# Kernel tuning notes

Hardware: AMD Instinct MI355X
Metric: run time of the kernel (lower is better)

The kernel has to match this reference:

```python
import jax, jax.numpy as jnp
import numpy as np

ALPHA, BETA, GAMMA, DELTA = 1.0, 1.0, 1.0, 0.001
DV, DD = 0.5, 1.5
N_INST = 8
EDGES_MAX = 512
EPS = 1e-12


def _safe_norm(sq):
    # sqrt of a sum-of-squares with a tiny eps for grad stability at 0
    return jnp.sqrt(jnp.maximum(sq, 0.0) + EPS)


def _per_image(feat, labels, label_edges):
    # feat: [P, C]; labels, label_edges: [P] int32 in [0, N_INST)
    P, C = feat.shape
    N = N_INST
    counts = jax.ops.segment_sum(jnp.ones((P,), feat.dtype), labels, num_segments=N)  # [N]
    means = jax.ops.segment_sum(feat, labels, num_segments=N) / counts[:, None]       # [N, C]

    # --- variance (pull) loss: per-pixel distance to its cluster mean ---
    d = _safe_norm(jnp.sum((feat - means[labels]) ** 2, axis=-1))  # [P]
    hinge = jax.nn.relu(d - DV) ** 2
    var_loss = jnp.sum(jax.ops.segment_sum(hinge, labels, num_segments=N) / counts) / N

    # --- distance (push) loss between cluster means, upper triangle ---
    diff = means[:, None, :] - means[None, :, :]
    dm = _safe_norm(jnp.sum(diff ** 2, axis=-1))  # [N, N]
    triu = jnp.triu(jnp.ones((N, N), dtype=bool), k=1)
    dist_loss = jnp.sum(jnp.where(triu, jax.nn.relu(2.0 * DD - dm) ** 2, 0.0)) / (N * (N - 1))

    # --- edge loss: first EDGES_MAX boundary pixels per instance (deterministic subsample) ---
    pix = jnp.arange(P, dtype=feat.dtype)
    def first_members(i):
        score = jnp.where(label_edges == i, -pix, -jnp.inf)
        _, idx = jax.lax.top_k(score, EDGES_MAX)
        return idx
    sel = jax.vmap(first_members)(jnp.arange(N))  # [N, E]
    eb = feat[sel.reshape(-1)]                    # [N*E, C]
    sq = jnp.sum(eb ** 2, axis=-1)
    d2 = sq[:, None] + sq[None, :] - 2.0 * (eb @ eb.T)  # [N*E, N*E] squared dists
    pd = _safe_norm(d2)
    pv = jax.nn.relu(2.0 * (DD - DV) - pd) ** 2
    pair = pv.reshape(N, EDGES_MAX, N, EDGES_MAX).sum(axis=(1, 3)) / (EDGES_MAX * EDGES_MAX)
    edge_loss = jnp.sum(jnp.where(triu, pair, 0.0)) / (N * (N - 1))

    # --- regularization on cluster means ---
    reg_loss = jnp.mean(_safe_norm(jnp.sum(means ** 2, axis=-1)))
    return var_loss, dist_loss, edge_loss, reg_loss


def setup_inputs() -> dict:
    key = jax.random.key(0)
    k1, k2, k3 = jax.random.split(key, 3)
    B, C, H, W = 4, 32, 512, 512
    features = jax.random.normal(k1, (B, C, H, W), jnp.float32)
    labels = jax.random.randint(k2, (B, H, W), 0, N_INST, jnp.int32)
    labelEdges = jax.random.randint(k3, (B, H, W), 0, N_INST, jnp.int32)
    return {"features": features, "labels": labels, "labelEdges": labelEdges}


def reference(features, labels, labelEdges):
    B, C, H, W = features.shape
    feat = features.transpose(0, 2, 3, 1).reshape(B, H * W, C)
    lab = labels.reshape(B, -1)
    le = labelEdges.reshape(B, -1)
    v, d, e, r = jax.vmap(_per_image)(feat, lab, le)
    varLoss = ALPHA * jnp.sum(v)
    distLoss = BETA * jnp.sum(d)
    edgeLoss = GAMMA * jnp.sum(e)
    regLoss = DELTA * jnp.sum(r)
    totalLoss = varLoss + distLoss + edgeLoss + regLoss
    return (totalLoss, varLoss, distLoss, edgeLoss, regLoss)
```

## Files before the change

### kernel.cpp

```cpp
#include <hip/hip_runtime.h>

#define NB 4
#define NC 32
#define NPIX 262144
#define NI 8
#define NE 512
#define FEPS 1e-12f
#define NSH 8

#define WS_SUMS   0
#define WS_HINGE  1056
#define WS_EDGE   1088
#define WS_PSUM   1152
#define WS_PCNT   9344
#define WS_ZERO_N 9600
#define WS_SEL    10240
#define WS_EB     28672
#define WS_SQ     294912

typedef __bf16 bf16x8 __attribute__((ext_vector_type(8)));
typedef float  f32x4  __attribute__((ext_vector_type(4)));

static __device__ __forceinline__ unsigned short f2bf(float x) {
    unsigned u = __builtin_bit_cast(unsigned, x);
    u += 0x7FFF + ((u >> 16) & 1);
    return (unsigned short)(u >> 16);
}

__global__ __launch_bounds__(256) void k_zero(float* __restrict__ ws) {
    int i = blockIdx.x * 256 + threadIdx.x;
    if (i < WS_ZERO_N) ws[i] = 0.f;
}

__global__ __launch_bounds__(256, 4) void k_seg_sums(const float* __restrict__ feat,
                                                     const int* __restrict__ lab,
                                                     float* __restrict__ psums,
                                                     float* __restrict__ pcnts) {
    __shared__ float sred[4][NI][33];
    __shared__ float cred[4][NI];
    int tid = threadIdx.x, lane = tid & 63, w = tid >> 6;
    int blk = blockIdx.x;
    int b = blk >> 9, chunk = blk & 511;
    int p0 = chunk * 512 + w * 128;
    int kg = lane >> 4, rc = lane & 15;
    const int* lb = lab + (size_t)b * NPIX;
    const float* f0 = feat + ((size_t)b * NC + rc) * NPIX;
    const float* f1 = feat + ((size_t)b * NC + 16 + rc) * NPIX;

    f32x4 acc0 = {0.f, 0.f, 0.f, 0.f}, acc1 = {0.f, 0.f, 0.f, 0.f};
    float cnt = 0.f;

#pragma unroll 2
    for (int it = 0; it < 4; it++) {
        int p = p0 + it * 32 + kg * 8;
        int4 la = *(const int4*)(lb + p);
        int4 lc = *(const int4*)(lb + p + 4);
        float4 a0 = *(const float4*)(f0 + p);
        float4 a1 = *(const float4*)(f0 + p + 4);
        float4 b0 = *(const float4*)(f1 + p);
        float4 b1 = *(const float4*)(f1 + p + 4);

        uint4 mu;
        mu.x = (la.x == rc ? 0x3F80u : 0u) | (la.y == rc ? 0x3F800000u : 0u);
        mu.y = (la.z == rc ? 0x3F80u : 0u) | (la.w == rc ? 0x3F800000u : 0u);
        mu.z = (lc.x == rc ? 0x3F80u : 0u) | (lc.y == rc ? 0x3F800000u : 0u);
        mu.w = (lc.z == rc ? 0x3F80u : 0u) | (lc.w == rc ? 0x3F800000u : 0u);
        cnt += (float)((la.x == rc) + (la.y == rc) + (la.z == rc) + (la.w == rc)
                     + (lc.x == rc) + (lc.y == rc) + (lc.z == rc) + (lc.w == rc));
        bf16x8 af = __builtin_bit_cast(bf16x8, mu);
        bf16x8 bf0 = {(__bf16)a0.x, (__bf16)a0.y, (__bf16)a0.z, (__bf16)a0.w,
                      (__bf16)a1.x, (__bf16)a1.y, (__bf16)a1.z, (__bf16)a1.w};
        bf16x8 bf1 = {(__bf16)b0.x, (__bf16)b0.y, (__bf16)b0.z, (__bf16)b0.w,
                      (__bf16)b1.x, (__bf16)b1.y, (__bf16)b1.z, (__bf16)b1.w};
        acc0 = __builtin_amdgcn_mfma_f32_16x16x32_bf16(af, bf0, acc0, 0, 0, 0);
        acc1 = __builtin_amdgcn_mfma_f32_16x16x32_bf16(af, bf1, acc1, 0, 0, 0);
    }

    if (lane < 32) {
#pragma unroll
        for (int rg = 0; rg < 4; rg++) {
            int row = (lane >> 4) * 4 + rg;
            sred[w][row][rc] = acc0[rg];
            sred[w][row][16 + rc] = acc1[rg];
        }
    }
    cnt += __shfl_xor(cnt, 16);
    cnt += __shfl_xor(cnt, 32);
    if (lane < 8) cred[w][lane] = cnt;
    __syncthreads();

    int sh = blk & (NSH - 1);
    {
        int bin = tid >> 5, ch = tid & 31;
        float s = sred[0][bin][ch] + sred[1][bin][ch] + sred[2][bin][ch] + sred[3][bin][ch];
        atomicAdd(&psums[sh * (NB * NI * NC) + ((size_t)b * NI + bin) * NC + ch], s);
    }
    if (tid < 8)
        atomicAdd(&pcnts[sh * (NB * NI) + b * NI + tid],
                  cred[0][tid] + cred[1][tid] + cred[2][tid] + cred[3][tid]);
}

__global__ __launch_bounds__(256, 4) void k_var(const float* __restrict__ feat,
                                                const int* __restrict__ lab,
                                                const float* __restrict__ psums,
                                                const float* __restrict__ pcnts,
                                                float* __restrict__ hinge) {
    __shared__ float mlds[NI][33];
    __shared__ float hred[4][8];
    int tid = threadIdx.x, lane = tid & 63, w = tid >> 6;
    int blk = blockIdx.x;
    int b = blk >> 9, chunk = blk & 511;
    {
        int bin = tid >> 5, ch = tid & 31;
        float s = 0.f, c = 0.f;
#pragma unroll
        for (int sh = 0; sh < NSH; sh++) {
            s += psums[sh * (NB * NI * NC) + ((size_t)b * NI + bin) * NC + ch];
            c += pcnts[sh * (NB * NI) + b * NI + bin];
        }
        mlds[bin][ch] = s / c;
    }
    __syncthreads();

    int p0 = chunk * 512 + tid * 2;
    int2 lv = *(const int2*)(lab + (size_t)b * NPIX + p0);
    const float* fb = feat + (size_t)b * NC * NPIX + p0;
    float a0 = 0.f, a1 = 0.f;
#pragma unroll
    for (int c = 0; c < NC; c++) {
        float2 f = *(const float2*)(fb + (size_t)c * NPIX);
        float d0 = f.x - mlds[lv.x][c]; a0 += d0 * d0;
        float d1 = f.y - mlds[lv.y][c]; a1 += d1 * d1;
    }
    float t;
    t = fmaxf(sqrtf(a0 + FEPS) - 0.5f, 0.f); float h0 = t * t;
    t = fmaxf(sqrtf(a1 + FEPS) - 0.5f, 0.f); float h1 = t * t;

    float hacc[8];
#pragma unroll
    for (int bin = 0; bin < 8; bin++)
        hacc[bin] = ((lv.x == bin) ? h0 : 0.f) + ((lv.y == bin) ? h1 : 0.f);
#pragma unroll
    for (int m = 8; m <= 32; m <<= 1) {
#pragma unroll
        for (int bin = 0; bin < 8; bin++) hacc[bin] += __shfl_xor(hacc[bin], m);
    }
#pragma unroll
    for (int half = 4; half >= 1; half >>= 1) {
#pragma unroll
        for (int k = 0; k < half; k++) {
            float t0 = __shfl_xor(hacc[k], half);
            float t1 = __shfl_xor(hacc[k + half], half);
            hacc[k] = (lane & half) ? (hacc[k + half] + t1) : (hacc[k] + t0);
        }
    }
    if (lane < 8) hred[w][lane] = hacc[0];
    __syncthreads();
    if (tid < 8)
        atomicAdd(&hinge[b * NI + tid],
                  hred[0][tid] + hred[1][tid] + hred[2][tid] + hred[3][tid]);
}

__global__ __launch_bounds__(64) void k_sel(const int* __restrict__ le, int* __restrict__ sel) {
    int inst = blockIdx.x & 7;
    int b = blockIdx.x >> 3;
    int lane = threadIdx.x;
    const int* lp = le + (size_t)b * NPIX;
    int* sp = sel + blockIdx.x * NE;
    int s = 0;
    for (int base = 0; base < NPIX && s < NE; base += 256) {
        int4 l = *(const int4*)(lp + base + lane * 4);
        int m0 = (l.x == inst), m1 = (l.y == inst), m2 = (l.z == inst), m3 = (l.w == inst);
        int cnt = m0 + m1 + m2 + m3;
        int incl = cnt;
#pragma unroll
        for (int off = 1; off < 64; off <<= 1) {
            int t = __shfl_up(incl, off);
            if (lane >= off) incl += t;
        }
        int r = incl - cnt;
        int pbase = base + lane * 4;
        if (m0) { if (s + r < NE) sp[s + r] = pbase + 0; r++; }
        if (m1) { if (s + r < NE) sp[s + r] = pbase + 1; r++; }
        if (m2) { if (s + r < NE) sp[s + r] = pbase + 2; r++; }
        if (m3) { if (s + r < NE) sp[s + r] = pbase + 3; r++; }
        s += __shfl(incl, 63);
    }
    for (int idx = s + lane; idx < NE; idx += 64) sp[idx] = 0;
}

__global__ __launch_bounds__(256) void k_gather(const float* __restrict__ feat,
                                                const int* __restrict__ sel,
                                                short* __restrict__ ebh,
                                                float* __restrict__ sq) {
    int oct = blockIdx.x;
    int bi = blockIdx.y;
    int b = bi >> 3;
    int tid = threadIdx.x;
    int rrel = tid >> 2, qc = tid & 3;
    int r = bi * NE + oct * 64 + rrel;
    int p = sel[r];
    const float* fp = feat + (size_t)b * NC * NPIX + p;
    int c0 = qc * 8;
    float s = 0.f;
    int pk[4];
#pragma unroll
    for (int j = 0; j < 4; j++) {
        float v0 = fp[(size_t)(c0 + 2 * j) * NPIX];
        float v1 = fp[(size_t)(c0 + 2 * j + 1) * NPIX];
        s += v0 * v0 + v1 * v1;
        pk[j] = (unsigned)f2bf(v0) | ((unsigned)f2bf(v1) << 16);
    }
    *(int4*)(ebh + (size_t)r * NC + c0) = make_int4(pk[0], pk[1], pk[2], pk[3]);
    s += __shfl_xor(s, 1);
    s += __shfl_xor(s, 2);
    if (qc == 0) sq[r] = s;
}

__global__ __launch_bounds__(256) void k_edge(const short* __restrict__ ebh,
                                              const float* __restrict__ sq,
                                              float* __restrict__ edge_acc) {
    __shared__ float sqa[128], sqb[128];
    __shared__ float wsum[4];
    int tid = threadIdx.x;
    int lane = tid & 63, w = tid >> 6;
    int ti = blockIdx.x >> 2, tj = blockIdx.x & 3;
    int q = blockIdx.y;
    int b = blockIdx.z;
    int pi = 0, pj = 0, k = q;
    for (int i = 0; i < 8; i++) { int row = 7 - i; if (k < row) { pi = i; pj = i + 1 + k; break; } k -= row; }
    int base_a = b * 4096 + pi * NE + ti * 128;
    int base_b = b * 4096 + pj * NE + tj * 128;

    if (tid < 128) sqa[tid] = sq[base_a + tid];
    else sqb[tid - 128] = sq[base_b + tid - 128];
    __syncthreads();

    int lrow = lane & 15;
    int lk = (lane >> 4) * 8;

    bf16x8 a[2];
#pragma unroll
    for (int u = 0; u < 2; u++)
        a[u] = *(const bf16x8*)(ebh + (size_t)(base_a + w * 32 + u * 16 + lrow) * NC + lk);
    bf16x8 bb[8];
#pragma unroll
    for (int v = 0; v < 8; v++)
        bb[v] = *(const bf16x8*)(ebh + (size_t)(base_b + v * 16 + lrow) * NC + lk);

    f32x4 acc[2][8];
#pragma unroll
    for (int u = 0; u < 2; u++)
#pragma unroll
        for (int v = 0; v < 8; v++) acc[u][v] = (f32x4){0.f, 0.f, 0.f, 0.f};

#pragma unroll
    for (int u = 0; u < 2; u++)
#pragma unroll
        for (int v = 0; v < 8; v++)
            acc[u][v] = __builtin_amdgcn_mfma_f32_16x16x32_bf16(a[u], bb[v], acc[u][v], 0, 0, 0);

    float lsum = 0.f;
    int orow0 = w * 32 + (lane >> 4) * 4;
    int ocol = lane & 15;
#pragma unroll
    for (int u = 0; u < 2; u++) {
#pragma unroll
        for (int v = 0; v < 8; v++) {
            float sb = sqb[v * 16 + ocol];
#pragma unroll
            for (int rg = 0; rg < 4; rg++) {
                float d2 = sqa[orow0 + u * 16 + rg] + sb - 2.f * acc[u][v][rg];
                float pd = sqrtf(fmaxf(d2, 0.f) + FEPS);
                float t = 2.f - pd;
                if (t > 0.f) lsum += t * t;
            }
        }
    }
#pragma unroll
    for (int off = 32; off > 0; off >>= 1) lsum += __shfl_xor(lsum, off);
    if (lane == 0) wsum[w] = lsum;
    __syncthreads();
    if (tid == 0) atomicAdd(edge_acc, wsum[0] + wsum[1] + wsum[2] + wsum[3]);
}

__global__ __launch_bounds__(256) void k_final(const float* __restrict__ psums,
                                               const float* __restrict__ pcnts,
                                               const float* __restrict__ hinge,
                                               const float* __restrict__ edge_acc,
                                               float* __restrict__ out) {
    __shared__ float m[NB * NI * NC];
    __shared__ float cshr[NB * NI];
    __shared__ float accs[3];
    int tid = threadIdx.x;
    if (tid < 3) accs[tid] = 0.f;
    if (tid < NB * NI) {
        float c = 0.f;
#pragma unroll
        for (int sh = 0; sh < NSH; sh++) c += pcnts[sh * (NB * NI) + tid];
        cshr[tid] = c;
    }
    __syncthreads();
    for (int i = tid; i < NB * NI * NC; i += 256) {
        float s = 0.f;
#pragma unroll
        for (int sh = 0; sh < NSH; sh++) s += psums[sh * (NB * NI * NC) + i];
        m[i] = s / cshr[i >> 5];
    }
    __syncthreads();

    float var_p = 0.f, dist_p = 0.f, reg_p = 0.f;
    if (tid < 32) {
        var_p = hinge[tid] / cshr[tid] * (1.f / 8.f);
        const float* mm = &m[tid * NC];
        float s = 0.f;
        for (int c = 0; c < NC; c++) s += mm[c] * mm[c];
        reg_p = sqrtf(s + FEPS) * (0.001f / 8.f);
    }
    if (tid < NB * 28) {
        int b = tid / 28, q = tid % 28;
        int pi = 0, pj = 0, k = q;
        for (int i = 0; i < 8; i++) { int row = 7 - i; if (k < row) { pi = i; pj = i + 1 + k; break; } k -= row; }
        const float* ma = &m[(b * NI + pi) * NC];
        const float* mb = &m[(b * NI + pj) * NC];
        float s = 0.f;
        for (int c = 0; c < NC; c++) { float d = ma[c] - mb[c]; s += d * d; }
        float dm = sqrtf(s + FEPS);
        float t = fmaxf(3.0f - dm, 0.f);
        dist_p = t * t * (1.f / 56.f);
    }
    atomicAdd(&accs[0], var_p);
    atomicAdd(&accs[1], dist_p);
    atomicAdd(&accs[2], reg_p);
    __syncthreads();
    if (tid == 0) {
        float var = accs[0], dist = accs[1], reg = accs[2];
        float edge = edge_acc[0] * (1.f / (512.f * 512.f * 56.f));
        out[0] = var + dist + edge + reg;
        out[1] = var;
        out[2] = dist;
        out[3] = edge;
        out[4] = reg;
    }
}

extern "C" void kernel_launch(void* const* d_in, const int* in_sizes, int n_in,
                              void* d_out, int out_size, void* d_ws, size_t ws_size,
                              hipStream_t stream) {
    const float* feat   = (const float*)d_in[0];
    const int*   labels = (const int*)d_in[1];
    const int*   le     = (const int*)d_in[2];
    float* out = (float*)d_out;
    float* ws  = (float*)d_ws;

    float* hinge = ws + WS_HINGE;
    float* edge  = ws + WS_EDGE;
    float* psums = ws + WS_PSUM;
    float* pcnts = ws + WS_PCNT;
    int*   sel   = (int*)(ws + WS_SEL);
    short* ebh   = (short*)(ws + WS_EB);
    float* sq    = ws + WS_SQ;

    hipLaunchKernelGGL(k_zero,     dim3(38),          dim3(256), 0, stream, ws);
    hipLaunchKernelGGL(k_seg_sums, dim3(2048),        dim3(256), 0, stream, feat, labels, psums, pcnts);
    hipLaunchKernelGGL(k_var,      dim3(2048),        dim3(256), 0, stream, feat, labels, psums, pcnts, hinge);
    hipLaunchKernelGGL(k_sel,      dim3(32),          dim3(64),  0, stream, le, sel);
    hipLaunchKernelGGL(k_gather,   dim3(8, 32),       dim3(256), 0, stream, feat, sel, ebh, sq);
    hipLaunchKernelGGL(k_edge,     dim3(16, 28, 4),   dim3(256), 0, stream, ebh, sq, edge);
    hipLaunchKernelGGL(k_final,    dim3(1),           dim3(256), 0, stream, psums, pcnts, hinge, edge, out);
}
```

Before: 286.9 us.

## Stage feature tiles into LDS via global_load_lds in segment-sum and variance kernels

Both streaming kernels now issue all their feature loads up front as direct global-to-LDS 16-byte transfers, then read the tile back from shared memory. Block size in pixels is halved and the grid doubled, so more loads are in flight per CU and the L2/HBM streams are better coalesced. In exchange each block uses 32KB of extra LDS, which may cap occupancy, and everything waits on a single vmcnt(0) with no overlap inside the block.

```diff
diff --git a/kernel.cpp b/kernel.cpp
--- a/kernel.cpp
+++ b/kernel.cpp
@@ -8,7 +8,6 @@
 #define FEPS 1e-12f
 #define NSH 8
 
-#define WS_SUMS   0
 #define WS_HINGE  1056
 #define WS_EDGE   1088
 #define WS_PSUM   1152
@@ -27,6 +26,13 @@
     return (unsigned short)(u >> 16);
 }
 
+static __device__ __forceinline__ void gload16(const float* g, float* l) {
+    __builtin_amdgcn_global_load_lds(
+        (const __attribute__((address_space(1))) void*)g,
+        (__attribute__((address_space(3))) void*)l,
+        16, 0, 0);
+}
+
 __global__ __launch_bounds__(256) void k_zero(float* __restrict__ ws) {
     int i = blockIdx.x * 256 + threadIdx.x;
     if (i < WS_ZERO_N) ws[i] = 0.f;
@@ -36,30 +42,35 @@
                                                      const int* __restrict__ lab,
                                                      float* __restrict__ psums,
                                                      float* __restrict__ pcnts) {
+    __shared__ float stg[4][2048];
     __shared__ float sred[4][NI][33];
     __shared__ float cred[4][NI];
     int tid = threadIdx.x, lane = tid & 63, w = tid >> 6;
     int blk = blockIdx.x;
-    int b = blk >> 9, chunk = blk & 511;
-    int p0 = chunk * 512 + w * 128;
+    int b = blk >> 10;
+    int p0 = (blk & 1023) * 256 + w * 64;
     int kg = lane >> 4, rc = lane & 15;
-    const int* lb = lab + (size_t)b * NPIX;
-    const float* f0 = feat + ((size_t)b * NC + rc) * NPIX;
-    const float* f1 = feat + ((size_t)b * NC + 16 + rc) * NPIX;
+
+    const float* fb = feat + (size_t)b * NC * NPIX;
+    const float* gp = fb + (size_t)(lane & 31) * NPIX + p0 + (lane >> 5) * 4;
+    float* lp = &stg[w][0];
+#pragma unroll
+    for (int g = 0; g < 8; g++) gload16(gp + g * 8, lp + g * 256);
+
+    const int* lb = lab + (size_t)b * NPIX + p0 + kg * 8;
+    int4 la0 = *(const int4*)(lb);
+    int4 lc0 = *(const int4*)(lb + 4);
+    int4 la1 = *(const int4*)(lb + 32);
+    int4 lc1 = *(const int4*)(lb + 36);
+
+    asm volatile("s_waitcnt vmcnt(0)" ::: "memory");
 
     f32x4 acc0 = {0.f, 0.f, 0.f, 0.f}, acc1 = {0.f, 0.f, 0.f, 0.f};
     float cnt = 0.f;
-
-#pragma unroll 2
-    for (int it = 0; it < 4; it++) {
-        int p = p0 + it * 32 + kg * 8;
-        int4 la = *(const int4*)(lb + p);
-        int4 lc = *(const int4*)(lb + p + 4);
-        float4 a0 = *(const float4*)(f0 + p);
-        float4 a1 = *(const float4*)(f0 + p + 4);
-        float4 b0 = *(const float4*)(f1 + p);
-        float4 b1 = *(const float4*)(f1 + p + 4);
-
+#pragma unroll
+    for (int ks = 0; ks < 2; ks++) {
+        int4 la = ks ? la1 : la0;
+        int4 lc = ks ? lc1 : lc0;
         uint4 mu;
         mu.x = (la.x == rc ? 0x3F80u : 0u) | (la.y == rc ? 0x3F800000u : 0u);
         mu.y = (la.z == rc ? 0x3F80u : 0u) | (la.w == rc ? 0x3F800000u : 0u);
@@ -68,10 +79,15 @@
         cnt += (float)((la.x == rc) + (la.y == rc) + (la.z == rc) + (la.w == rc)
                      + (lc.x == rc) + (lc.y == rc) + (lc.z == rc) + (lc.w == rc));
         bf16x8 af = __builtin_bit_cast(bf16x8, mu);
-        bf16x8 bf0 = {(__bf16)a0.x, (__bf16)a0.y, (__bf16)a0.z, (__bf16)a0.w,
-                      (__bf16)a1.x, (__bf16)a1.y, (__bf16)a1.z, (__bf16)a1.w};
-        bf16x8 bf1 = {(__bf16)b0.x, (__bf16)b0.y, (__bf16)b0.z, (__bf16)b0.w,
-                      (__bf16)b1.x, (__bf16)b1.y, (__bf16)b1.z, (__bf16)b1.w};
+        const float* c0 = lp + (ks * 8 + kg * 2) * 128 + rc * 4;
+        float4 x0 = *(const float4*)(c0);
+        float4 x1 = *(const float4*)(c0 + 128);
+        float4 y0 = *(const float4*)(c0 + 64);
+        float4 y1 = *(const float4*)(c0 + 192);
+        bf16x8 bf0 = {(__bf16)x0.x, (__bf16)x0.y, (__bf16)x0.z, (__bf16)x0.w,
+                      (__bf16)x1.x, (__bf16)x1.y, (__bf16)x1.z, (__bf16)x1.w};
+        bf16x8 bf1 = {(__bf16)y0.x, (__bf16)y0.y, (__bf16)y0.z, (__bf16)y0.w,
+                      (__bf16)y1.x, (__bf16)y1.y, (__bf16)y1.z, (__bf16)y1.w};
         acc0 = __builtin_amdgcn_mfma_f32_16x16x32_bf16(af, bf0, acc0, 0, 0, 0);
         acc1 = __builtin_amdgcn_mfma_f32_16x16x32_bf16(af, bf1, acc1, 0, 0, 0);
     }
@@ -105,11 +121,14 @@
                                                 const float* __restrict__ psums,
                                                 const float* __restrict__ pcnts,
                                                 float* __restrict__ hinge) {
+    __shared__ float stg[4][2048];
     __shared__ float mlds[NI][33];
     __shared__ float hred[4][8];
     int tid = threadIdx.x, lane = tid & 63, w = tid >> 6;
     int blk = blockIdx.x;
-    int b = blk >> 9, chunk = blk & 511;
+    int b = blk >> 10;
+    int p0 = (blk & 1023) * 256 + w * 64;
+
     {
         int bin = tid >> 5, ch = tid & 31;
         float s = 0.f, c = 0.f;
@@ -122,24 +141,28 @@
     }
     __syncthreads();
 
-    int p0 = chunk * 512 + tid * 2;
-    int2 lv = *(const int2*)(lab + (size_t)b * NPIX + p0);
-    const float* fb = feat + (size_t)b * NC * NPIX + p0;
-    float a0 = 0.f, a1 = 0.f;
+    const float* gp = feat + (size_t)b * NC * NPIX + (size_t)(lane >> 4) * NPIX
+                    + p0 + (lane & 15) * 4;
+    float* lp = &stg[w][0];
+#pragma unroll
+    for (int g = 0; g < 8; g++) gload16(gp + (size_t)g * 4 * NPIX, lp + g * 256);
+
+    int lv = lab[(size_t)b * NPIX + p0 + lane];
+
+    asm volatile("s_waitcnt vmcnt(0)" ::: "memory");
+
+    float a0 = 0.f;
 #pragma unroll
     for (int c = 0; c < NC; c++) {
-        float2 f = *(const float2*)(fb + (size_t)c * NPIX);
-        float d0 = f.x - mlds[lv.x][c]; a0 += d0 * d0;
-        float d1 = f.y - mlds[lv.y][c]; a1 += d1 * d1;
-    }
-    float t;
-    t = fmaxf(sqrtf(a0 + FEPS) - 0.5f, 0.f); float h0 = t * t;
-    t = fmaxf(sqrtf(a1 + FEPS) - 0.5f, 0.f); float h1 = t * t;
+        float d = lp[c * 64 + lane] - mlds[lv][c];
+        a0 += d * d;
+    }
+    float t = fmaxf(sqrtf(a0 + FEPS) - 0.5f, 0.f);
+    float h0 = t * t;
 
     float hacc[8];
 #pragma unroll
-    for (int bin = 0; bin < 8; bin++)
-        hacc[bin] = ((lv.x == bin) ? h0 : 0.f) + ((lv.y == bin) ? h1 : 0.f);
+    for (int bin = 0; bin < 8; bin++) hacc[bin] = (lv == bin) ? h0 : 0.f;
 #pragma unroll
     for (int m = 8; m <= 32; m <<= 1) {
 #pragma unroll
@@ -362,8 +385,8 @@
     float* sq    = ws + WS_SQ;
 
     hipLaunchKernelGGL(k_zero,     dim3(38),          dim3(256), 0, stream, ws);
-    hipLaunchKernelGGL(k_seg_sums, dim3(2048),        dim3(256), 0, stream, feat, labels, psums, pcnts);
-    hipLaunchKernelGGL(k_var,      dim3(2048),        dim3(256), 0, stream, feat, labels, psums, pcnts, hinge);
+    hipLaunchKernelGGL(k_seg_sums, dim3(4096),        dim3(256), 0, stream, feat, labels, psums, pcnts);
+    hipLaunchKernelGGL(k_var,      dim3(4096),        dim3(256), 0, stream, feat, labels, psums, pcnts, hinge);
     hipLaunchKernelGGL(k_sel,      dim3(32),          dim3(64),  0, stream, le, sel);
     hipLaunchKernelGGL(k_gather,   dim3(8, 32),       dim3(256), 0, stream, feat, sel, ebh, sq);
     hipLaunchKernelGGL(k_edge,     dim3(16, 28, 4),   dim3(256), 0, stream, ebh, sq, edge);
```

After: 310.3 us. +8.2%, slower.
